# Optimization experiments

Measured on AMD Instinct MI355X. Metric: run time of the kernel, lower is better.

Reference implementation:

```python
import jax, jax.numpy as jnp
import numpy as np

N_EMBED = 384
NUM_EXPERTS = 8
TOP_K = 2


def setup_inputs() -> dict:
    key = jax.random.key(0)
    k_x, k_n, k_w1, k_b1, k_w2, k_b2 = jax.random.split(key, 6)
    B, T = 16, 4096
    bound = 1.0 / np.sqrt(N_EMBED)
    return {
        "x": jax.random.normal(k_x, (B, T, N_EMBED), dtype=jnp.float32),
        "noise": jax.random.normal(k_n, (B, T, NUM_EXPERTS), dtype=jnp.float32),
        "w_route": jax.random.uniform(k_w1, (NUM_EXPERTS, N_EMBED), jnp.float32, -bound, bound),
        "b_route": jax.random.uniform(k_b1, (NUM_EXPERTS,), jnp.float32, -bound, bound),
        "w_noise": jax.random.uniform(k_w2, (NUM_EXPERTS, N_EMBED), jnp.float32, -bound, bound),
        "b_noise": jax.random.uniform(k_b2, (NUM_EXPERTS,), jnp.float32, -bound, bound),
    }


def reference(x, noise, w_route, b_route, w_noise, b_noise):
    # two tiny linears: [B,T,D] @ [D,E] -> [B,T,E]
    logits = jnp.einsum("btd,ed->bte", x, w_route) + b_route
    noise_logits = jnp.einsum("btd,ed->bte", x, w_noise) + b_noise
    noisy_logits = logits + noise * jax.nn.softplus(noise_logits)

    top_k_logits, indices = jax.lax.top_k(noisy_logits, TOP_K)  # [B,T,k]

    # scatter top-k values into a -inf tensor; equivalently mask non-topk to -inf
    # (values at the top-k positions are exactly the noisy logits there)
    mask = jax.nn.one_hot(indices, NUM_EXPERTS, dtype=jnp.bool_).any(axis=-2)  # [B,T,E]
    sparse_logits = jnp.where(mask, noisy_logits, -jnp.inf)
    router_output = jax.nn.softmax(sparse_logits, axis=-1)
    return router_output, indices
```

## Files before the change

kernel.cpp:

```cpp
#include <hip/hip_runtime.h>
#include <math.h>


constexpr int D = 384;

__device__ __forceinline__ float dpp_xor1(float v) {
    return __int_as_float(__builtin_amdgcn_update_dpp(
        0, __float_as_int(v), 0xB1, 0xF, 0xF, true));
}
__device__ __forceinline__ float dpp_xor2(float v) {
    return __int_as_float(__builtin_amdgcn_update_dpp(
        0, __float_as_int(v), 0x4E, 0xF, 0xF, true));
}
__device__ __forceinline__ float swz_xor4(float v) {
    return __int_as_float(__builtin_amdgcn_ds_swizzle(__float_as_int(v), 0x101F));
}

__global__ __launch_bounds__(256, 4) void noisy_topk_router_f32(
    const float* __restrict__ x,
    const float* __restrict__ noise,
    const float* __restrict__ w_route,
    const float* __restrict__ b_route,
    const float* __restrict__ w_noise,
    const float* __restrict__ b_noise,
    float* __restrict__ out,
    int ntok)
{
    __shared__ float w_lds[16 * D];
    __shared__ float bias[16];

    const int tid = threadIdx.x;

#pragma unroll
    for (int r = 0; r < 3; ++r) {
        int i = (tid + 256 * r) * 4;
        *(float4*)(w_lds + i)        = *(const float4*)(w_route + i);
        *(float4*)(w_lds + 3072 + i) = *(const float4*)(w_noise + i);
    }
    if (tid < 8)       bias[tid] = b_route[tid];
    else if (tid < 16) bias[tid] = b_noise[tid - 8];
    __syncthreads();

    const int wave = tid >> 6;
    const int lane = tid & 63;
    const int tg   = lane >> 3;
    const int c    = lane & 7;
    const int tok0 = blockIdx.x * 64 + wave * 16 + tg * 2;

    float acc[2][16];
#pragma unroll
    for (int t = 0; t < 2; ++t)
#pragma unroll
        for (int e = 0; e < 16; ++e) acc[t][e] = 0.f;

    const float* xr = x + (size_t)tok0 * D + c * 4;

    float4 xa[2][3], xb[2][3];
#pragma unroll
    for (int qq = 0; qq < 3; ++qq) {
        xa[0][qq] = *(const float4*)(xr + qq * 32);
        xa[1][qq] = *(const float4*)(xr + D + qq * 32);
    }

#pragma unroll
    for (int s = 0; s < 4; ++s) {
        const int qn = (s < 3) ? (s + 1) * 3 : 0;
#pragma unroll
        for (int qq = 0; qq < 3; ++qq) {
            xb[0][qq] = *(const float4*)(xr + (qn + qq) * 32);
            xb[1][qq] = *(const float4*)(xr + D + (qn + qq) * 32);
        }
#pragma unroll
        for (int qq = 0; qq < 3; ++qq) {
            const int q = s * 3 + qq;
            const float* wj = w_lds + q * 32 + c * 4;
#pragma unroll
            for (int e = 0; e < 16; ++e) {
                float4 wv = *(const float4*)(wj + e * D);
                acc[0][e] += xa[0][qq].x * wv.x + xa[0][qq].y * wv.y
                           + xa[0][qq].z * wv.z + xa[0][qq].w * wv.w;
                acc[1][e] += xa[1][qq].x * wv.x + xa[1][qq].y * wv.y
                           + xa[1][qq].z * wv.z + xa[1][qq].w * wv.w;
            }
        }
#pragma unroll
        for (int qq = 0; qq < 3; ++qq) {
            xa[0][qq] = xb[0][qq];
            xa[1][qq] = xb[1][qq];
        }
    }

    const bool b0 = (c & 1);
    float a1[16];
#pragma unroll
    for (int e = 0; e < 16; ++e) {
        float s = b0 ? acc[0][e] : acc[1][e];
        float k = b0 ? acc[1][e] : acc[0][e];
        a1[e] = k + dpp_xor1(s);
    }
#pragma unroll
    for (int e = 0; e < 16; ++e) a1[e] += dpp_xor2(a1[e]);
#pragma unroll
    for (int e = 0; e < 16; ++e) a1[e] += swz_xor4(a1[e]);

    if (c < 2) {
        const int token = tok0 + c;
        float4 n0 = *(const float4*)(noise + (size_t)token * 8);
        float4 n1 = *(const float4*)(noise + (size_t)token * 8 + 4);
        float nz[8] = {n0.x, n0.y, n0.z, n0.w, n1.x, n1.y, n1.z, n1.w};

        float noisy[8];
#pragma unroll
        for (int e = 0; e < 8; ++e) {
            float lg = a1[e] + bias[e];
            float nl = a1[8 + e] + bias[8 + e];
            float sp = fmaxf(nl, 0.f) + log1pf(expf(-fabsf(nl)));
            noisy[e] = lg + nz[e] * sp;
        }

        float v0 = noisy[0]; int i0 = 0;
#pragma unroll
        for (int e = 1; e < 8; ++e)
            if (noisy[e] > v0) { v0 = noisy[e]; i0 = e; }
        float v1 = -INFINITY; int i1 = 0;
#pragma unroll
        for (int e = 0; e < 8; ++e)
            if (e != i0 && noisy[e] > v1) { v1 = noisy[e]; i1 = e; }

        float ex  = expf(v1 - v0);
        float inv = 1.f / (1.f + ex);
        float p0  = inv;
        float p1  = ex * inv;

        float pr[8];
#pragma unroll
        for (int e = 0; e < 8; ++e)
            pr[e] = (e == i0) ? p0 : ((e == i1) ? p1 : 0.f);

        float* orow = out + (size_t)token * 8;
        *(float4*)(orow)     = make_float4(pr[0], pr[1], pr[2], pr[3]);
        *(float4*)(orow + 4) = make_float4(pr[4], pr[5], pr[6], pr[7]);

        *(float2*)(out + (size_t)ntok * 8 + (size_t)token * 2) =
            make_float2((float)i0, (float)i1);
    }
}

extern "C" void kernel_launch(void* const* d_in, const int* in_sizes, int n_in,
                              void* d_out, int out_size, void* d_ws, size_t ws_size,
                              hipStream_t stream) {
    const float* x       = (const float*)d_in[0];
    const float* noise   = (const float*)d_in[1];
    const float* w_route = (const float*)d_in[2];
    const float* b_route = (const float*)d_in[3];
    const float* w_noise = (const float*)d_in[4];
    const float* b_noise = (const float*)d_in[5];
    float* out = (float*)d_out;

    const int ntok   = in_sizes[0] / D;
    const int blocks = ntok / 64;

    hipLaunchKernelGGL(noisy_topk_router_f32, dim3(blocks), dim3(256), 0, stream,
                       x, noise, w_route, b_route, w_noise, b_noise, out, ntok);
}
```

Measured before the change: 163.8 us.

## Use nontemporal loads/stores, issue x loads before weight LDS staging, drop redundant prefetch

Streaming traffic (x, noise, outputs) now goes through nontemporal loads and stores so it is not kept in cache. The first x tile loads are issued alongside the global weight loads, before the LDS writes and barrier, so their latency overlaps the weight staging. The last loop iteration no longer issues a wasted reload of the first x chunk. This trades some register pressure for fewer stalls and less cache traffic on a memory-bound kernel.

```diff
diff --git a/kernel.cpp b/kernel.cpp
--- a/kernel.cpp
+++ b/kernel.cpp
@@ -3,6 +3,22 @@
 
 
 constexpr int D = 384;
+
+typedef float vfloat4 __attribute__((ext_vector_type(4)));
+typedef float vfloat2 __attribute__((ext_vector_type(2)));
+
+__device__ __forceinline__ float4 ntload4(const float* p) {
+    vfloat4 v = __builtin_nontemporal_load((const vfloat4*)p);
+    return make_float4(v.x, v.y, v.z, v.w);
+}
+__device__ __forceinline__ void ntstore4(float* p, float4 v) {
+    vfloat4 t = {v.x, v.y, v.z, v.w};
+    __builtin_nontemporal_store(t, (vfloat4*)p);
+}
+__device__ __forceinline__ void ntstore2(float* p, float2 v) {
+    vfloat2 t = {v.x, v.y};
+    __builtin_nontemporal_store(t, (vfloat2*)p);
+}
 
 __device__ __forceinline__ float dpp_xor1(float v) {
     return __int_as_float(__builtin_amdgcn_update_dpp(
@@ -31,21 +47,38 @@
 
     const int tid = threadIdx.x;
 
-#pragma unroll
-    for (int r = 0; r < 3; ++r) {
-        int i = (tid + 256 * r) * 4;
-        *(float4*)(w_lds + i)        = *(const float4*)(w_route + i);
-        *(float4*)(w_lds + 3072 + i) = *(const float4*)(w_noise + i);
-    }
-    if (tid < 8)       bias[tid] = b_route[tid];
-    else if (tid < 16) bias[tid] = b_noise[tid - 8];
-    __syncthreads();
-
     const int wave = tid >> 6;
     const int lane = tid & 63;
     const int tg   = lane >> 3;
     const int c    = lane & 7;
     const int tok0 = blockIdx.x * 64 + wave * 16 + tg * 2;
+
+    const float* xr = x + (size_t)tok0 * D + c * 4;
+
+    float4 wr[3], wn[3];
+    int widx[3];
+#pragma unroll
+    for (int r = 0; r < 3; ++r) {
+        widx[r] = (tid + 256 * r) * 4;
+        wr[r] = *(const float4*)(w_route + widx[r]);
+        wn[r] = *(const float4*)(w_noise + widx[r]);
+    }
+
+    float4 xa[2][3], xb[2][3];
+#pragma unroll
+    for (int qq = 0; qq < 3; ++qq) {
+        xa[0][qq] = ntload4(xr + qq * 32);
+        xa[1][qq] = ntload4(xr + D + qq * 32);
+    }
+
+#pragma unroll
+    for (int r = 0; r < 3; ++r) {
+        *(float4*)(w_lds + widx[r])        = wr[r];
+        *(float4*)(w_lds + 3072 + widx[r]) = wn[r];
+    }
+    if (tid < 8)       bias[tid] = b_route[tid];
+    else if (tid < 16) bias[tid] = b_noise[tid - 8];
+    __syncthreads();
 
     float acc[2][16];
 #pragma unroll
@@ -53,22 +86,15 @@
 #pragma unroll
         for (int e = 0; e < 16; ++e) acc[t][e] = 0.f;
 
-    const float* xr = x + (size_t)tok0 * D + c * 4;
-
-    float4 xa[2][3], xb[2][3];
-#pragma unroll
-    for (int qq = 0; qq < 3; ++qq) {
-        xa[0][qq] = *(const float4*)(xr + qq * 32);
-        xa[1][qq] = *(const float4*)(xr + D + qq * 32);
-    }
-
 #pragma unroll
     for (int s = 0; s < 4; ++s) {
-        const int qn = (s < 3) ? (s + 1) * 3 : 0;
+        if (s < 3) {
+            const int qn = (s + 1) * 3;
 #pragma unroll
-        for (int qq = 0; qq < 3; ++qq) {
-            xb[0][qq] = *(const float4*)(xr + (qn + qq) * 32);
-            xb[1][qq] = *(const float4*)(xr + D + (qn + qq) * 32);
+            for (int qq = 0; qq < 3; ++qq) {
+                xb[0][qq] = ntload4(xr + (qn + qq) * 32);
+                xb[1][qq] = ntload4(xr + D + (qn + qq) * 32);
+            }
         }
 #pragma unroll
         for (int qq = 0; qq < 3; ++qq) {
@@ -83,10 +109,12 @@
                            + xa[1][qq].z * wv.z + xa[1][qq].w * wv.w;
             }
         }
+        if (s < 3) {
 #pragma unroll
-        for (int qq = 0; qq < 3; ++qq) {
-            xa[0][qq] = xb[0][qq];
-            xa[1][qq] = xb[1][qq];
+            for (int qq = 0; qq < 3; ++qq) {
+                xa[0][qq] = xb[0][qq];
+                xa[1][qq] = xb[1][qq];
+            }
         }
     }
 
@@ -105,8 +133,8 @@
 
     if (c < 2) {
         const int token = tok0 + c;
-        float4 n0 = *(const float4*)(noise + (size_t)token * 8);
-        float4 n1 = *(const float4*)(noise + (size_t)token * 8 + 4);
+        float4 n0 = ntload4(noise + (size_t)token * 8);
+        float4 n1 = ntload4(noise + (size_t)token * 8 + 4);
         float nz[8] = {n0.x, n0.y, n0.z, n0.w, n1.x, n1.y, n1.z, n1.w};
 
         float noisy[8];
@@ -138,11 +166,11 @@
             pr[e] = (e == i0) ? p0 : ((e == i1) ? p1 : 0.f);
 
         float* orow = out + (size_t)token * 8;
-        *(float4*)(orow)     = make_float4(pr[0], pr[1], pr[2], pr[3]);
-        *(float4*)(orow + 4) = make_float4(pr[4], pr[5], pr[6], pr[7]);
+        ntstore4(orow,     make_float4(pr[0], pr[1], pr[2], pr[3]));
+        ntstore4(orow + 4, make_float4(pr[4], pr[5], pr[6], pr[7]));
 
-        *(float2*)(out + (size_t)ntok * 8 + (size_t)token * 2) =
-            make_float2((float)i0, (float)i1);
+        ntstore2(out + (size_t)ntok * 8 + (size_t)token * 2,
+                 make_float2((float)i0, (float)i1));
     }
 }
 
```

Result: slower. 167.9 us (+2.5%).

## Use packed FMA and 16 lanes per token pair, halving tokens per block

Applied to the files above, without the earlier changes.

Each token pair is now spread over 16 lanes instead of 8, so each block covers 32 tokens and the grid doubles. The dot products use v_pk_fma_f32 on two-wide float vectors, and an extra swizzle step is added to the cross-lane reduction. The explicit double-buffered prefetch of x is dropped in favour of a simple unrolled loop. The intent is more parallelism and fewer FMA instructions for a memory-bound kernel. The cost is more blocks each reloading the 24KB weight tile into LDS, plus an extra reduction stage.

```diff
diff --git a/kernel.cpp b/kernel.cpp
--- a/kernel.cpp
+++ b/kernel.cpp
@@ -3,6 +3,14 @@
 
 
 constexpr int D = 384;
+
+typedef float v2f __attribute__((ext_vector_type(2)));
+
+struct alignas(16) W2 { v2f lo, hi; };
+
+__device__ __forceinline__ void pk_fma(v2f& a, v2f b, v2f c) {
+    asm("v_pk_fma_f32 %0, %1, %2, %0" : "+v"(a) : "v"(b), "v"(c));
+}
 
 __device__ __forceinline__ float dpp_xor1(float v) {
     return __int_as_float(__builtin_amdgcn_update_dpp(
@@ -14,6 +22,9 @@
 }
 __device__ __forceinline__ float swz_xor4(float v) {
     return __int_as_float(__builtin_amdgcn_ds_swizzle(__float_as_int(v), 0x101F));
+}
+__device__ __forceinline__ float swz_xor8(float v) {
+    return __int_as_float(__builtin_amdgcn_ds_swizzle(__float_as_int(v), 0x201F));
 }
 
 __global__ __launch_bounds__(256, 4) void noisy_topk_router_f32(
@@ -43,65 +54,54 @@
 
     const int wave = tid >> 6;
     const int lane = tid & 63;
-    const int tg   = lane >> 3;
-    const int c    = lane & 7;
-    const int tok0 = blockIdx.x * 64 + wave * 16 + tg * 2;
+    const int g    = lane >> 4;
+    const int c    = lane & 15;
+    const int tok0 = blockIdx.x * 32 + wave * 8 + g * 2;
 
-    float acc[2][16];
+    v2f acc[2][16];
 #pragma unroll
     for (int t = 0; t < 2; ++t)
 #pragma unroll
-        for (int e = 0; e < 16; ++e) acc[t][e] = 0.f;
+        for (int e = 0; e < 16; ++e) acc[t][e] = (v2f)(0.f);
 
     const float* xr = x + (size_t)tok0 * D + c * 4;
 
-    float4 xa[2][3], xb[2][3];
 #pragma unroll
-    for (int qq = 0; qq < 3; ++qq) {
-        xa[0][qq] = *(const float4*)(xr + qq * 32);
-        xa[1][qq] = *(const float4*)(xr + D + qq * 32);
+    for (int q = 0; q < 6; ++q) {
+        W2 xt0 = *(const W2*)(xr + q * 64);
+        W2 xt1 = *(const W2*)(xr + q * 64 + D);
+        const float* wb = w_lds + q * 64 + c * 4;
+#pragma unroll
+        for (int e = 0; e < 16; ++e) {
+            W2 w = *(const W2*)(wb + e * D);
+            pk_fma(acc[0][e], xt0.lo, w.lo);
+            pk_fma(acc[0][e], xt0.hi, w.hi);
+            pk_fma(acc[1][e], xt1.lo, w.lo);
+            pk_fma(acc[1][e], xt1.hi, w.hi);
+        }
     }
 
+    float f0[16], f1[16];
 #pragma unroll
-    for (int s = 0; s < 4; ++s) {
-        const int qn = (s < 3) ? (s + 1) * 3 : 0;
-#pragma unroll
-        for (int qq = 0; qq < 3; ++qq) {
-            xb[0][qq] = *(const float4*)(xr + (qn + qq) * 32);
-            xb[1][qq] = *(const float4*)(xr + D + (qn + qq) * 32);
-        }
-#pragma unroll
-        for (int qq = 0; qq < 3; ++qq) {
-            const int q = s * 3 + qq;
-            const float* wj = w_lds + q * 32 + c * 4;
-#pragma unroll
-            for (int e = 0; e < 16; ++e) {
-                float4 wv = *(const float4*)(wj + e * D);
-                acc[0][e] += xa[0][qq].x * wv.x + xa[0][qq].y * wv.y
-                           + xa[0][qq].z * wv.z + xa[0][qq].w * wv.w;
-                acc[1][e] += xa[1][qq].x * wv.x + xa[1][qq].y * wv.y
-                           + xa[1][qq].z * wv.z + xa[1][qq].w * wv.w;
-            }
-        }
-#pragma unroll
-        for (int qq = 0; qq < 3; ++qq) {
-            xa[0][qq] = xb[0][qq];
-            xa[1][qq] = xb[1][qq];
-        }
+    for (int e = 0; e < 16; ++e) {
+        f0[e] = acc[0][e].x + acc[0][e].y;
+        f1[e] = acc[1][e].x + acc[1][e].y;
     }
 
     const bool b0 = (c & 1);
     float a1[16];
 #pragma unroll
     for (int e = 0; e < 16; ++e) {
-        float s = b0 ? acc[0][e] : acc[1][e];
-        float k = b0 ? acc[1][e] : acc[0][e];
+        float s = b0 ? f0[e] : f1[e];
+        float k = b0 ? f1[e] : f0[e];
         a1[e] = k + dpp_xor1(s);
     }
 #pragma unroll
     for (int e = 0; e < 16; ++e) a1[e] += dpp_xor2(a1[e]);
 #pragma unroll
     for (int e = 0; e < 16; ++e) a1[e] += swz_xor4(a1[e]);
+#pragma unroll
+    for (int e = 0; e < 16; ++e) a1[e] += swz_xor8(a1[e]);
 
     if (c < 2) {
         const int token = tok0 + c;
@@ -158,7 +158,7 @@
     float* out = (float*)d_out;
 
     const int ntok   = in_sizes[0] / D;
-    const int blocks = ntok / 64;
+    const int blocks = ntok / 32;
 
     hipLaunchKernelGGL(noisy_topk_router_f32, dim3(blocks), dim3(256), 0, stream,
                        x, noise, w_route, b_route, w_noise, b_noise, out, ntok);
```

Result: slower. 173.0 us (+5.6%).
